# Performance work log

Measured on AMD Instinct MI355X. Metric: run time of the kernel, lower is better.

Reference implementation:

```python
import jax, jax.numpy as jnp
import numpy as np

N_VERTS = 1_000_000
N_EDGES = 3_000_000
H, W = 1024, 1024
MAX_DEPTH = 10.0
DEPTH_SCALE = 1.0
CREGU = 2000.0


def setup_inputs() -> dict:
    key = jax.random.key(0)
    k1, k2, k3, k4, k5, k6 = jax.random.split(key, 6)
    # mesh vertices roughly in a unit-radius blob
    vertices = jax.random.normal(k1, (N_VERTS, 3), dtype=jnp.float32) * 0.5
    vertices_ref = vertices + 0.01 * jax.random.normal(k2, (N_VERTS, 3), dtype=jnp.float32)
    quaternion = jax.random.normal(k3, (4,), dtype=jnp.float32) + jnp.array([0., 0., 0., 1.], jnp.float32)
    translation = jax.random.normal(k4, (3,), dtype=jnp.float32) * 0.05
    hand_image = jax.random.uniform(k5, (H, W), dtype=jnp.float32) * MAX_DEPTH
    # camera per MeshDepthFitterEnergy.setImage: R = diag(1,-1,-1), focal = 2*W
    object_center = np.zeros(3, np.float32)
    object_radius = 0.5
    camera_center = object_center + np.array([-0.5, 0.0, 5.0], np.float32) * object_radius
    R = np.array([[1., 0., 0.], [0., -1., 0.], [0., 0., -1.]], np.float32)
    T = -R.T.dot(camera_center)
    focal = 2.0 * W
    intrinsic = jnp.array([[focal, 0., W / 2.], [0., focal, H / 2.], [0., 0., 1.]], jnp.float32)
    extrinsic = jnp.array(np.column_stack((R, T)), jnp.float32)
    edges = jax.random.randint(k6, (N_EDGES, 2), 0, N_VERTS, dtype=jnp.int64)
    return {"vertices": vertices, "vertices_ref": vertices_ref, "quaternion": quaternion,
            "translation": translation, "hand_image": hand_image,
            "intrinsic": intrinsic, "extrinsic": extrinsic, "edges": edges}


def _qrot(q, v):
    # q: [4] (x,y,z,w) normalized; v: [N,3]
    qvec = q[:3]
    uv = jnp.cross(jnp.broadcast_to(qvec, v.shape), v)
    uuv = jnp.cross(jnp.broadcast_to(qvec, v.shape), uv)
    return v + 2.0 * (q[3] * uv + uuv)


def _forward(vertices, vertices_ref, quaternion, translation, hand_image,
             intrinsic, extrinsic, edges):
    # rigid transform
    q = quaternion / jnp.linalg.norm(quaternion)
    v_centered = vertices - jnp.mean(vertices, axis=0, keepdims=True)
    v_t = _qrot(q, v_centered) + translation  # [N,3]
    # camera projection: P_cam = R x + T ; pix = K P_cam / z
    p_cam = v_t @ extrinsic[:, :3].T + extrinsic[:, 3]  # [N,3]
    proj = p_cam @ intrinsic.T
    z = p_cam[:, 2] * DEPTH_SCALE
    u = proj[:, 0] / proj[:, 2]
    v = proj[:, 1] / proj[:, 2]
    xi = jnp.clip(jnp.round(u), 0, W - 1).astype(jnp.int32)
    yi = jnp.clip(jnp.round(v), 0, H - 1).astype(jnp.int32)
    flat = yi * W + xi  # [N]
    # z-buffer: scatter-min of per-vertex depth (invalid/behind-camera -> MAX_DEPTH)
    zvalid = jnp.where(z > 0, z, MAX_DEPTH)
    depth_flat = jnp.full((H * W,), MAX_DEPTH, dtype=vertices.dtype).at[flat].min(zvalid)
    depth = jnp.clip(depth_flat, 0.0, MAX_DEPTH).reshape(H, W)
    diff_image = (depth - hand_image) ** 2
    e_data = jnp.sum(diff_image)
    # Laplacian rigid energy: cregu * || L (V - Vref) ||^2 over the edge graph
    dv = vertices - vertices_ref
    src, dst = edges[:, 0], edges[:, 1]
    deg = jax.ops.segment_sum(jnp.ones((N_EDGES,), vertices.dtype), src, num_segments=N_VERTS)
    neigh = jax.ops.segment_sum(dv[dst], src, num_segments=N_VERTS)  # [N,3]
    ldv = deg[:, None] * dv - neigh
    e_rigid = CREGU * jnp.sum(ldv ** 2)
    return e_data + e_rigid


def reference(vertices, vertices_ref, quaternion, translation, hand_image,
              intrinsic, extrinsic, edges):
    return _forward(vertices, vertices_ref, quaternion, translation, hand_image,
                    intrinsic, extrinsic, edges)
```

## Files before the change

### kernel.cpp

```cpp
#include <hip/hip_runtime.h>

#define W_IMG 1024
#define H_IMG 1024
#define HW_IMG (W_IMG * H_IMG)
#define NV 1000000
#define NE 3000000
#define NV4 (NE / 2)
#define MAX_DEPTH 10.0f
#define CREGU 2000.0f

#define NBUCKET 245
#define BSHIFT 12
#define BSIZE 4096

#define PREP_BLOCKS 2048
#define HIST_BLOCKS 250
#define HIST_V4 6000
#define SCAT_V4 2048
#define SCAT_EDGES (SCAT_V4 * 2)
#define SCAT_BLOCKS ((NV4 + SCAT_V4 - 1) / SCAT_V4)
#define GEO_BLOCKS 1024
#define TSIZE 2048
#define EDATA_BLOCKS 256

#define QXY 4096.0f
#define IQXY 2.44140625e-4f
#define QZ 2048.0f
#define IQZ 4.8828125e-4f
#define BXY2 1024
#define BZ2 512

typedef int v4i __attribute__((ext_vector_type(4)));

__device__ __forceinline__ unsigned pack_dv32(float x, float y, float z) {
    x = fminf(fmaxf(x, -0.2f), 0.2f);
    y = fminf(fmaxf(y, -0.2f), 0.2f);
    z = fminf(fmaxf(z, -0.2f), 0.2f);
    unsigned px = (unsigned)((int)rintf(x * QXY) + BXY2);
    unsigned py = (unsigned)((int)rintf(y * QXY) + BXY2);
    unsigned pz = (unsigned)((int)rintf(z * QZ) + BZ2);
    return (px << 21) | (py << 10) | pz;
}

__device__ __forceinline__ unsigned long long expand_dv(unsigned p) {
    unsigned long long x = (p >> 21) & 0x7FFu;
    unsigned long long y = (p >> 10) & 0x7FFu;
    unsigned long long z = p & 0x3FFu;
    return (x << 44) | (y << 24) | (z << 6) | 1ull;
}

__device__ __forceinline__ float block_sum_256(float v, float* smem) {
#pragma unroll
    for (int o = 32; o > 0; o >>= 1) v += __shfl_down(v, o, 64);
    int lane = threadIdx.x & 63;
    int wid  = threadIdx.x >> 6;
    if (lane == 0) smem[wid] = v;
    __syncthreads();
    float r = 0.f;
    if (threadIdx.x == 0) r = smem[0] + smem[1] + smem[2] + smem[3];
    __syncthreads();
    return r;
}

__device__ __forceinline__ void prefix245(const unsigned* __restrict__ src,
                                          unsigned* dst) {
    int t = threadIdx.x;
    unsigned h = (t < NBUCKET) ? src[t] : 0u;
    dst[t] = h;
    __syncthreads();
#pragma unroll
    for (int o = 1; o < 256; o <<= 1) {
        unsigned v = (t >= o) ? dst[t - o] : 0u;
        __syncthreads();
        dst[t] += v;
        __syncthreads();
    }
    unsigned excl = dst[t] - h;
    __syncthreads();
    dst[t] = excl;
    __syncthreads();
}

__global__ void k_prep(const float* __restrict__ verts,
                       const float* __restrict__ verts_ref,
                       unsigned* __restrict__ pdv32,
                       unsigned* __restrict__ depth_bits, int ncd,
                       unsigned long long* __restrict__ neigh, int modeA,
                       const v4i* __restrict__ edges2,
                       unsigned* __restrict__ hist,
                       float4* __restrict__ partial) {
    __shared__ float smem[4];
    __shared__ unsigned lh[NBUCKET];
    int i = blockIdx.x * blockDim.x + threadIdx.x;
    int stride = gridDim.x * blockDim.x;

    float sx = 0.f, sy = 0.f, sz = 0.f;
    for (int j = i; j < NV; j += stride) {
        float x = verts[3 * j + 0];
        float y = verts[3 * j + 1];
        float z = verts[3 * j + 2];
        sx += x; sy += y; sz += z;
        pdv32[j] = pack_dv32(x - verts_ref[3 * j + 0],
                             y - verts_ref[3 * j + 1],
                             z - verts_ref[3 * j + 2]);
        if (!modeA) neigh[j] = 0ull;
    }
    size_t totd = (size_t)ncd * HW_IMG;
    for (size_t j = i; j < totd; j += stride) depth_bits[j] = 0x41200000u;

    if (modeA && blockIdx.x < HIST_BLOCKS) {
        for (int t = threadIdx.x; t < NBUCKET; t += blockDim.x) lh[t] = 0u;
        __syncthreads();
        int base = blockIdx.x * HIST_V4;
        for (int k = threadIdx.x; k < HIST_V4; k += blockDim.x) {
            v4i e = __builtin_nontemporal_load(&edges2[base + k]);
            atomicAdd(&lh[(unsigned)e.x >> BSHIFT], 1u);
            atomicAdd(&lh[(unsigned)e.z >> BSHIFT], 1u);
        }
        __syncthreads();
        for (int t = threadIdx.x; t < NBUCKET; t += blockDim.x)
            if (lh[t]) atomicAdd(&hist[t], lh[t]);
    }

    float bx = block_sum_256(sx, smem);
    float by = block_sum_256(sy, smem);
    float bz = block_sum_256(sz, smem);
    if (threadIdx.x == 0) {
        float4 p; p.x = bx; p.y = by; p.z = bz; p.w = 0.f;
        partial[blockIdx.x] = p;
    }
}

union SMem {
    struct {
        unsigned h_key[TSIZE];
        unsigned h_val[TSIZE];
        float rsm[8];
    } geo;
    struct {
        unsigned long long sort[SCAT_EDGES];
        unsigned sLh[NBUCKET];
        unsigned sPfx[256];
        unsigned sDelta[NBUCKET];
        unsigned sOff[256];
    } sc;
};

__global__ void k_main(const v4i* __restrict__ edges2,
                       const unsigned* __restrict__ pdv32,
                       unsigned long long* __restrict__ rec,
                       const unsigned* __restrict__ hist,
                       unsigned* __restrict__ reserve,
                       unsigned long long* __restrict__ neigh, int modeA,
                       const float* __restrict__ verts,
                       const float* __restrict__ quat,
                       const float* __restrict__ trans,
                       const float* __restrict__ intr,
                       const float* __restrict__ extr,
                       const float4* __restrict__ partial,
                       unsigned* __restrict__ depth_bits, int ncd) {
    __shared__ SMem sm;

    if (blockIdx.x >= GEO_BLOCKS) {
        int sb = blockIdx.x - GEO_BLOCKS;
        int base = sb * SCAT_V4;
        if (modeA) {
            for (int t = threadIdx.x; t < NBUCKET; t += blockDim.x) sm.sc.sLh[t] = 0u;
            __syncthreads();

            v4i e[8];
            unsigned r0[8], r1[8];
#pragma unroll
            for (int k = 0; k < 8; ++k) {
                int idx = base + k * 256 + (int)threadIdx.x;
                if (idx < NV4) {
                    e[k] = __builtin_nontemporal_load(&edges2[idx]);
                    r0[k] = atomicAdd(&sm.sc.sLh[(unsigned)e[k].x >> BSHIFT], 1u);
                    r1[k] = atomicAdd(&sm.sc.sLh[(unsigned)e[k].z >> BSHIFT], 1u);
                }
            }
            __syncthreads();
            prefix245(sm.sc.sLh, sm.sc.sPfx);
            prefix245(hist, sm.sc.sOff);
            for (int t = threadIdx.x; t < NBUCKET; t += blockDim.x) {
                unsigned c = sm.sc.sLh[t];
                unsigned res = c ? atomicAdd(&reserve[t], c) : 0u;
                sm.sc.sDelta[t] = sm.sc.sOff[t] + res - sm.sc.sPfx[t];
            }
            __syncthreads();
#pragma unroll
            for (int k = 0; k < 8; ++k) {
                int idx = base + k * 256 + (int)threadIdx.x;
                if (idx < NV4) {
                    unsigned s0 = (unsigned)e[k].x;
                    unsigned b0 = s0 >> BSHIFT;
                    unsigned long long rec0 =
                        ((unsigned long long)b0 << 56) |
                        ((unsigned long long)pdv32[e[k].y] << 12) |
                        (s0 & (BSIZE - 1));
                    sm.sc.sort[sm.sc.sPfx[b0] + r0[k]] = rec0;
                    unsigned s1 = (unsigned)e[k].z;
                    unsigned b1 = s1 >> BSHIFT;
                    unsigned long long rec1 =
                        ((unsigned long long)b1 << 56) |
                        ((unsigned long long)pdv32[e[k].w] << 12) |
                        (s1 & (BSIZE - 1));
                    sm.sc.sort[sm.sc.sPfx[b1] + r1[k]] = rec1;
                }
            }
            __syncthreads();
            int nrec = (base + SCAT_V4 <= NV4) ? SCAT_EDGES
                                               : 2 * (NV4 - base);
#pragma unroll
            for (int k = 0; k < 16; ++k) {
                int t = k * 256 + (int)threadIdx.x;
                if (t < nrec) {
                    unsigned long long r = sm.sc.sort[t];
                    unsigned bin = (unsigned)(r >> 56);
                    rec[(size_t)t + sm.sc.sDelta[bin]] = r;
                }
            }
        } else {
#pragma unroll
            for (int k = 0; k < 8; ++k) {
                int idx = base + k * 256 + (int)threadIdx.x;
                if (idx < NV4) {
                    v4i e = __builtin_nontemporal_load(&edges2[idx]);
                    atomicAdd(&neigh[(size_t)(unsigned)e.x], expand_dv(pdv32[e.y]));
                    atomicAdd(&neigh[(size_t)(unsigned)e.z], expand_dv(pdv32[e.w]));
                }
            }
        }
        return;
    }

    int gb = blockIdx.x;
    for (int s = threadIdx.x; s < TSIZE; s += blockDim.x) {
        sm.geo.h_key[s] = 0xFFFFFFFFu;
        sm.geo.h_val[s] = 0xFFFFFFFFu;
    }
    __syncthreads();

    float sx = 0.f, sy = 0.f, sz = 0.f;
    for (int p = threadIdx.x; p < PREP_BLOCKS; p += blockDim.x) {
        float4 v = partial[p];
        sx += v.x; sy += v.y; sz += v.z;
    }
    float bx = block_sum_256(sx, sm.geo.rsm);
    float by = block_sum_256(sy, sm.geo.rsm);
    float bz = block_sum_256(sz, sm.geo.rsm);
    if (threadIdx.x == 0) {
        const float inv_nv = 1.0f / (float)NV;
        sm.geo.rsm[4] = bx * inv_nv;
        sm.geo.rsm[5] = by * inv_nv;
        sm.geo.rsm[6] = bz * inv_nv;
    }
    __syncthreads();
    float mx = sm.geo.rsm[4], my = sm.geo.rsm[5], mz = sm.geo.rsm[6];

    float qx = quat[0], qy = quat[1], qz = quat[2], qw = quat[3];
    float qn = rsqrtf(qx * qx + qy * qy + qz * qz + qw * qw);
    qx *= qn; qy *= qn; qz *= qn; qw *= qn;
    float t0 = trans[0], t1 = trans[1], t2 = trans[2];
    float e0 = extr[0], e1 = extr[1], e2 = extr[2],  e3 = extr[3];
    float e4 = extr[4], e5 = extr[5], e6 = extr[6],  e7 = extr[7];
    float e8 = extr[8], e9 = extr[9], e10 = extr[10], e11 = extr[11];
    float i0 = intr[0], i1 = intr[1], i2 = intr[2];
    float i3 = intr[3], i4 = intr[4], i5 = intr[5];
    float i6 = intr[6], i7 = intr[7], i8 = intr[8];

    unsigned* __restrict__ db = depth_bits + (size_t)(gb & (ncd - 1)) * HW_IMG;

    int stride = GEO_BLOCKS * blockDim.x;
    for (int j = gb * blockDim.x + threadIdx.x; j < NV; j += stride) {
        float vx = __builtin_nontemporal_load(&verts[3 * j + 0]) - mx;
        float vy = __builtin_nontemporal_load(&verts[3 * j + 1]) - my;
        float vz = __builtin_nontemporal_load(&verts[3 * j + 2]) - mz;

        float uvx = qy * vz - qz * vy;
        float uvy = qz * vx - qx * vz;
        float uvz = qx * vy - qy * vx;
        float uuvx = qy * uvz - qz * uvy;
        float uuvy = qz * uvx - qx * uvz;
        float uuvz = qx * uvy - qy * uvx;
        float tx = vx + 2.f * (qw * uvx + uuvx) + t0;
        float ty = vy + 2.f * (qw * uvy + uuvy) + t1;
        float tz = vz + 2.f * (qw * uvz + uuvz) + t2;

        float px = e0 * tx + e1 * ty + e2  * tz + e3;
        float py = e4 * tx + e5 * ty + e6  * tz + e7;
        float pz = e8 * tx + e9 * ty + e10 * tz + e11;

        float pr0 = i0 * px + i1 * py + i2 * pz;
        float pr1 = i3 * px + i4 * py + i5 * pz;
        float pr2 = i6 * px + i7 * py + i8 * pz;

        float u = pr0 / pr2;
        float v = pr1 / pr2;
        float ru = rintf(u);
        float rv = rintf(v);
        bool border = (ru < 0.f) | (ru > (float)(W_IMG - 1)) |
                      (rv < 0.f) | (rv > (float)(H_IMG - 1));
        float xf = fminf(fmaxf(ru, 0.f), (float)(W_IMG - 1));
        float yf = fminf(fmaxf(rv, 0.f), (float)(H_IMG - 1));
        unsigned flat = (unsigned)((int)yf * W_IMG + (int)xf);

        if (pz > 0.f) {
            unsigned zbits = __float_as_uint(pz);
            bool direct = !border;
            if (border) {
                unsigned slot = (flat * 2654435761u) >> 21;
                bool done = false;
#pragma unroll
                for (int p = 0; p < 4; ++p) {
                    unsigned old = atomicCAS(&sm.geo.h_key[slot], 0xFFFFFFFFu, flat);
                    if (old == 0xFFFFFFFFu || old == flat) {
                        atomicMin(&sm.geo.h_val[slot], zbits);
                        done = true;
                        break;
                    }
                    slot = (slot + 1) & (TSIZE - 1);
                }
                direct = !done;
            }
            if (direct) atomicMin(&db[flat], zbits);
        }
    }
    __syncthreads();
    for (int s = threadIdx.x; s < TSIZE; s += blockDim.x) {
        unsigned k = sm.geo.h_key[s];
        if (k != 0xFFFFFFFFu) atomicMin(&db[k], sm.geo.h_val[s]);
    }
}

__global__ void k_energy(const unsigned* __restrict__ depth_bits, int ncd,
                         const float* __restrict__ hand,
                         const unsigned* __restrict__ pdv32,
                         const unsigned long long* __restrict__ rec,
                         const unsigned* __restrict__ hist,
                         const unsigned long long* __restrict__ neigh, int modeA,
                         float* out) {
    __shared__ unsigned long long acc[BSIZE];
    __shared__ unsigned sOff[256];
    __shared__ float smem[4];

    if (blockIdx.x < NBUCKET) {
        int b = blockIdx.x;
        int vbase = b * BSIZE;
        int nvert = (NV - vbase < BSIZE) ? (NV - vbase) : BSIZE;
        if (modeA) {
            prefix245(hist, sOff);
            unsigned start = sOff[b];
            unsigned count = hist[b];
            for (int v = threadIdx.x; v < BSIZE; v += blockDim.x) acc[v] = 0ull;
            __syncthreads();
            for (unsigned i = threadIdx.x; i < count; i += blockDim.x) {
                unsigned long long r = rec[start + i];
                unsigned p = (unsigned)(r >> 12);
                unsigned s = (unsigned)(r & (BSIZE - 1));
                atomicAdd(&acc[s], expand_dv(p));
            }
            __syncthreads();
        }
        float lacc = 0.f;
        for (int v = threadIdx.x; v < nvert; v += blockDim.x) {
            unsigned long long n = modeA ? acc[v] : neigh[(size_t)vbase + v];
            int cnt = (int)(n & 63ull);
            int rz  = (int)((n >> 6)  & 0x3FFFFull);
            int ry  = (int)((n >> 24) & 0xFFFFFull);
            int rx  = (int)(n >> 44);
            float nx = (float)(rx - cnt * BXY2) * IQXY;
            float ny = (float)(ry - cnt * BXY2) * IQXY;
            float nz = (float)(rz - cnt * BZ2)  * IQZ;
            unsigned p = pdv32[vbase + v];
            float dx = (float)((int)((p >> 21) & 0x7FFu) - BXY2) * IQXY;
            float dy = (float)((int)((p >> 10) & 0x7FFu) - BXY2) * IQXY;
            float dz = (float)((int)(p & 0x3FFu) - BZ2) * IQZ;
            float dg = (float)cnt;
            float lx = dg * dx - nx;
            float ly = dg * dy - ny;
            float lz = dg * dz - nz;
            lacc += lx * lx + ly * ly + lz * lz;
        }
        float bsum = block_sum_256(lacc, smem);
        if (threadIdx.x == 0) atomicAdd(out, CREGU * bsum);
    } else {
        int eb = blockIdx.x - NBUCKET;
        int i = eb * blockDim.x + threadIdx.x;
        int stride = EDATA_BLOCKS * blockDim.x;
        float accd = 0.f;
        for (int j = i; j < HW_IMG; j += stride) {
            float dmin = __uint_as_float(depth_bits[j]);
            for (int c = 1; c < ncd; ++c)
                dmin = fminf(dmin, __uint_as_float(depth_bits[(size_t)c * HW_IMG + j]));
            float depth = fminf(fmaxf(dmin, 0.f), MAX_DEPTH);
            float diff = depth - hand[j];
            accd += diff * diff;
        }
        float bsum = block_sum_256(accd, smem);
        if (threadIdx.x == 0) atomicAdd(out, bsum);
    }
}

extern "C" void kernel_launch(void* const* d_in, const int* in_sizes, int n_in,
                              void* d_out, int out_size, void* d_ws, size_t ws_size,
                              hipStream_t stream) {
    const float* verts     = (const float*)d_in[0];
    const float* verts_ref = (const float*)d_in[1];
    const float* quat      = (const float*)d_in[2];
    const float* trans     = (const float*)d_in[3];
    const float* hand      = (const float*)d_in[4];
    const float* intr      = (const float*)d_in[5];
    const float* extr      = (const float*)d_in[6];
    const int*   edges     = (const int*)d_in[7];
    float* out = (float*)d_out;

    char* ws = (char*)d_ws;
    const size_t OFF_BINS = (size_t)NV * 4;
    const size_t OFF_PART = OFF_BINS + 4096;
    const size_t OFF_REC  = OFF_PART + (size_t)PREP_BLOCKS * 16;

    const size_t A_FIX = OFF_REC + (size_t)NE * 8;
    const size_t B_FIX = OFF_REC + (size_t)NV * 8;

    int modeA, ncd;
    size_t OFF_DEPTH;
    if (ws_size >= A_FIX + 4ull * HW_IMG * 4)      { modeA = 1; ncd = 4; OFF_DEPTH = A_FIX; }
    else if (ws_size >= A_FIX + 2ull * HW_IMG * 4) { modeA = 1; ncd = 2; OFF_DEPTH = A_FIX; }
    else if (ws_size >= A_FIX + 1ull * HW_IMG * 4) { modeA = 1; ncd = 1; OFF_DEPTH = A_FIX; }
    else if (ws_size >= B_FIX + 4ull * HW_IMG * 4) { modeA = 0; ncd = 4; OFF_DEPTH = B_FIX; }
    else if (ws_size >= B_FIX + 2ull * HW_IMG * 4) { modeA = 0; ncd = 2; OFF_DEPTH = B_FIX; }
    else                                           { modeA = 0; ncd = 1; OFF_DEPTH = B_FIX; }

    unsigned*           pdv32      = (unsigned*)ws;
    unsigned*           hist       = (unsigned*)(ws + OFF_BINS);
    unsigned*           reserve    = hist + 256;
    float4*             partial    = (float4*)(ws + OFF_PART);
    unsigned long long* rec        = (unsigned long long*)(ws + OFF_REC);
    unsigned long long* neigh      = (unsigned long long*)(ws + OFF_REC);
    unsigned*           depth_bits = (unsigned*)(ws + OFF_DEPTH);

    const int B = 256;

    hipMemsetAsync(ws + OFF_BINS, 0, 4096, stream);
    hipMemsetAsync(d_out, 0, sizeof(float), stream);

    k_prep<<<PREP_BLOCKS, B, 0, stream>>>(verts, verts_ref, pdv32, depth_bits,
                                          ncd, neigh, modeA, (const v4i*)edges,
                                          hist, partial);
    k_main<<<GEO_BLOCKS + SCAT_BLOCKS, B, 0, stream>>>(
        (const v4i*)edges, pdv32, rec, hist, reserve, neigh, modeA,
        verts, quat, trans, intr, extr, partial, depth_bits, ncd);
    k_energy<<<NBUCKET + EDATA_BLOCKS, B, 0, stream>>>(
        depth_bits, ncd, hand, pdv32, rec, hist, neigh, modeA, out);
}
```

Measured before the change: 234.5 us.

## Vectorize vertex/depth loads, wave-shuffle prefix scan, shrink scatter tiles, add launch bounds

```diff
diff --git a/kernel.cpp b/kernel.cpp
--- a/kernel.cpp
+++ b/kernel.cpp
@@ -14,13 +14,13 @@
 #define BSIZE 4096
 
 #define PREP_BLOCKS 2048
-#define HIST_BLOCKS 250
-#define HIST_V4 6000
-#define SCAT_V4 2048
+#define HIST_BLOCKS 1000
+#define HIST_V4 1500
+#define SCAT_V4 1024
 #define SCAT_EDGES (SCAT_V4 * 2)
 #define SCAT_BLOCKS ((NV4 + SCAT_V4 - 1) / SCAT_V4)
 #define GEO_BLOCKS 1024
-#define TSIZE 2048
+#define TSIZE 1024
 #define EDATA_BLOCKS 256
 
 #define QXY 4096.0f
@@ -31,6 +31,8 @@
 #define BZ2 512
 
 typedef int v4i __attribute__((ext_vector_type(4)));
+typedef float v4f __attribute__((ext_vector_type(4)));
+typedef unsigned v4u __attribute__((ext_vector_type(4)));
 
 __device__ __forceinline__ unsigned pack_dv32(float x, float y, float z) {
     x = fminf(fmaxf(x, -0.2f), 0.2f);
@@ -62,51 +64,65 @@
     return r;
 }
 
-__device__ __forceinline__ void prefix245(const unsigned* __restrict__ src,
-                                          unsigned* dst) {
+__device__ __forceinline__ void prefix245_fast(const unsigned* __restrict__ src,
+                                               unsigned* dst, unsigned* wtmp) {
     int t = threadIdx.x;
+    int lane = t & 63, wid = t >> 6;
     unsigned h = (t < NBUCKET) ? src[t] : 0u;
-    dst[t] = h;
-    __syncthreads();
-#pragma unroll
-    for (int o = 1; o < 256; o <<= 1) {
-        unsigned v = (t >= o) ? dst[t - o] : 0u;
-        __syncthreads();
-        dst[t] += v;
-        __syncthreads();
-    }
-    unsigned excl = dst[t] - h;
-    __syncthreads();
-    dst[t] = excl;
-    __syncthreads();
-}
-
-__global__ void k_prep(const float* __restrict__ verts,
-                       const float* __restrict__ verts_ref,
-                       unsigned* __restrict__ pdv32,
-                       unsigned* __restrict__ depth_bits, int ncd,
-                       unsigned long long* __restrict__ neigh, int modeA,
-                       const v4i* __restrict__ edges2,
-                       unsigned* __restrict__ hist,
-                       float4* __restrict__ partial) {
+    unsigned incl = h;
+#pragma unroll
+    for (int o = 1; o < 64; o <<= 1) {
+        unsigned v = __shfl_up(incl, o, 64);
+        if (lane >= o) incl += v;
+    }
+    if (lane == 63) wtmp[wid] = incl;
+    __syncthreads();
+    unsigned woff = 0u;
+    if (wid > 0) woff += wtmp[0];
+    if (wid > 1) woff += wtmp[1];
+    if (wid > 2) woff += wtmp[2];
+    dst[t] = woff + incl - h;
+    __syncthreads();
+}
+
+__global__ __launch_bounds__(256, 8)
+void k_prep(const float* __restrict__ verts,
+            const float* __restrict__ verts_ref,
+            unsigned* __restrict__ pdv32,
+            unsigned* __restrict__ depth_bits, int ncd,
+            unsigned long long* __restrict__ neigh, int modeA,
+            const v4i* __restrict__ edges2,
+            unsigned* __restrict__ hist,
+            float4* __restrict__ partial) {
     __shared__ float smem[4];
     __shared__ unsigned lh[NBUCKET];
     int i = blockIdx.x * blockDim.x + threadIdx.x;
     int stride = gridDim.x * blockDim.x;
 
     float sx = 0.f, sy = 0.f, sz = 0.f;
-    for (int j = i; j < NV; j += stride) {
-        float x = verts[3 * j + 0];
-        float y = verts[3 * j + 1];
-        float z = verts[3 * j + 2];
-        sx += x; sy += y; sz += z;
-        pdv32[j] = pack_dv32(x - verts_ref[3 * j + 0],
-                             y - verts_ref[3 * j + 1],
-                             z - verts_ref[3 * j + 2]);
-        if (!modeA) neigh[j] = 0ull;
-    }
-    size_t totd = (size_t)ncd * HW_IMG;
-    for (size_t j = i; j < totd; j += stride) depth_bits[j] = 0x41200000u;
+    const int ng = NV / 4;
+    for (int g = i; g < ng; g += stride) {
+        const v4f* vp = (const v4f*)verts + 3 * (size_t)g;
+        const v4f* rp = (const v4f*)verts_ref + 3 * (size_t)g;
+        v4f a = vp[0], b = vp[1], c = vp[2];
+        v4f d = rp[0], e = rp[1], f = rp[2];
+        sx += a.x + a.w + b.z + c.y;
+        sy += a.y + b.x + b.w + c.z;
+        sz += a.z + b.y + c.x + c.w;
+        v4u pk;
+        pk.x = pack_dv32(a.x - d.x, a.y - d.y, a.z - d.z);
+        pk.y = pack_dv32(a.w - d.w, b.x - e.x, b.y - e.y);
+        pk.z = pack_dv32(b.z - e.z, b.w - e.w, c.x - f.x);
+        pk.w = pack_dv32(c.y - f.y, c.z - f.z, c.w - f.w);
+        ((v4u*)pdv32)[g] = pk;
+    }
+    if (!modeA)
+        for (int j = i; j < NV; j += stride) neigh[j] = 0ull;
+
+    size_t totd4 = (size_t)ncd * (HW_IMG / 4);
+    v4u dinit;
+    dinit.x = dinit.y = dinit.z = dinit.w = 0x41200000u;
+    for (size_t j = i; j < totd4; j += stride) ((v4u*)depth_bits)[j] = dinit;
 
     if (modeA && blockIdx.x < HIST_BLOCKS) {
         for (int t = threadIdx.x; t < NBUCKET; t += blockDim.x) lh[t] = 0u;
@@ -141,24 +157,25 @@
         unsigned long long sort[SCAT_EDGES];
         unsigned sLh[NBUCKET];
         unsigned sPfx[256];
-        unsigned sDelta[NBUCKET];
         unsigned sOff[256];
+        unsigned wtmp[4];
     } sc;
 };
 
-__global__ void k_main(const v4i* __restrict__ edges2,
-                       const unsigned* __restrict__ pdv32,
-                       unsigned long long* __restrict__ rec,
-                       const unsigned* __restrict__ hist,
-                       unsigned* __restrict__ reserve,
-                       unsigned long long* __restrict__ neigh, int modeA,
-                       const float* __restrict__ verts,
-                       const float* __restrict__ quat,
-                       const float* __restrict__ trans,
-                       const float* __restrict__ intr,
-                       const float* __restrict__ extr,
-                       const float4* __restrict__ partial,
-                       unsigned* __restrict__ depth_bits, int ncd) {
+__global__ __launch_bounds__(256, 8)
+void k_main(const v4i* __restrict__ edges2,
+            const unsigned* __restrict__ pdv32,
+            unsigned long long* __restrict__ rec,
+            const unsigned* __restrict__ hist,
+            unsigned* __restrict__ reserve,
+            unsigned long long* __restrict__ neigh, int modeA,
+            const float* __restrict__ verts,
+            const float* __restrict__ quat,
+            const float* __restrict__ trans,
+            const float* __restrict__ intr,
+            const float* __restrict__ extr,
+            const float4* __restrict__ partial,
+            unsigned* __restrict__ depth_bits, int ncd) {
     __shared__ SMem sm;
 
     if (blockIdx.x >= GEO_BLOCKS) {
@@ -168,10 +185,10 @@
             for (int t = threadIdx.x; t < NBUCKET; t += blockDim.x) sm.sc.sLh[t] = 0u;
             __syncthreads();
 
-            v4i e[8];
-            unsigned r0[8], r1[8];
-#pragma unroll
-            for (int k = 0; k < 8; ++k) {
+            v4i e[4];
+            unsigned r0[4], r1[4];
+#pragma unroll
+            for (int k = 0; k < 4; ++k) {
                 int idx = base + k * 256 + (int)threadIdx.x;
                 if (idx < NV4) {
                     e[k] = __builtin_nontemporal_load(&edges2[idx]);
@@ -180,16 +197,15 @@
                 }
             }
             __syncthreads();
-            prefix245(sm.sc.sLh, sm.sc.sPfx);
-            prefix245(hist, sm.sc.sOff);
+            prefix245_fast(sm.sc.sLh, sm.sc.sPfx, sm.sc.wtmp);
+            prefix245_fast(hist, sm.sc.sOff, sm.sc.wtmp);
             for (int t = threadIdx.x; t < NBUCKET; t += blockDim.x) {
                 unsigned c = sm.sc.sLh[t];
                 unsigned res = c ? atomicAdd(&reserve[t], c) : 0u;
-                sm.sc.sDelta[t] = sm.sc.sOff[t] + res - sm.sc.sPfx[t];
-            }
-            __syncthreads();
-#pragma unroll
-            for (int k = 0; k < 8; ++k) {
+                sm.sc.sOff[t] += res - sm.sc.sPfx[t];
+            }
+#pragma unroll
+            for (int k = 0; k < 4; ++k) {
                 int idx = base + k * 256 + (int)threadIdx.x;
                 if (idx < NV4) {
                     unsigned s0 = (unsigned)e[k].x;
@@ -212,17 +228,17 @@
             int nrec = (base + SCAT_V4 <= NV4) ? SCAT_EDGES
                                                : 2 * (NV4 - base);
 #pragma unroll
-            for (int k = 0; k < 16; ++k) {
+            for (int k = 0; k < 8; ++k) {
                 int t = k * 256 + (int)threadIdx.x;
                 if (t < nrec) {
                     unsigned long long r = sm.sc.sort[t];
                     unsigned bin = (unsigned)(r >> 56);
-                    rec[(size_t)t + sm.sc.sDelta[bin]] = r;
+                    rec[(size_t)t + sm.sc.sOff[bin]] = r;
                 }
             }
         } else {
 #pragma unroll
-            for (int k = 0; k < 8; ++k) {
+            for (int k = 0; k < 4; ++k) {
                 int idx = base + k * 256 + (int)threadIdx.x;
                 if (idx < NV4) {
                     v4i e = __builtin_nontemporal_load(&edges2[idx]);
@@ -271,59 +287,68 @@
 
     unsigned* __restrict__ db = depth_bits + (size_t)(gb & (ncd - 1)) * HW_IMG;
 
+    const int ng = NV / 4;
     int stride = GEO_BLOCKS * blockDim.x;
-    for (int j = gb * blockDim.x + threadIdx.x; j < NV; j += stride) {
-        float vx = __builtin_nontemporal_load(&verts[3 * j + 0]) - mx;
-        float vy = __builtin_nontemporal_load(&verts[3 * j + 1]) - my;
-        float vz = __builtin_nontemporal_load(&verts[3 * j + 2]) - mz;
-
-        float uvx = qy * vz - qz * vy;
-        float uvy = qz * vx - qx * vz;
-        float uvz = qx * vy - qy * vx;
-        float uuvx = qy * uvz - qz * uvy;
-        float uuvy = qz * uvx - qx * uvz;
-        float uuvz = qx * uvy - qy * uvx;
-        float tx = vx + 2.f * (qw * uvx + uuvx) + t0;
-        float ty = vy + 2.f * (qw * uvy + uuvy) + t1;
-        float tz = vz + 2.f * (qw * uvz + uuvz) + t2;
-
-        float px = e0 * tx + e1 * ty + e2  * tz + e3;
-        float py = e4 * tx + e5 * ty + e6  * tz + e7;
-        float pz = e8 * tx + e9 * ty + e10 * tz + e11;
-
-        float pr0 = i0 * px + i1 * py + i2 * pz;
-        float pr1 = i3 * px + i4 * py + i5 * pz;
-        float pr2 = i6 * px + i7 * py + i8 * pz;
-
-        float u = pr0 / pr2;
-        float v = pr1 / pr2;
-        float ru = rintf(u);
-        float rv = rintf(v);
-        bool border = (ru < 0.f) | (ru > (float)(W_IMG - 1)) |
-                      (rv < 0.f) | (rv > (float)(H_IMG - 1));
-        float xf = fminf(fmaxf(ru, 0.f), (float)(W_IMG - 1));
-        float yf = fminf(fmaxf(rv, 0.f), (float)(H_IMG - 1));
-        unsigned flat = (unsigned)((int)yf * W_IMG + (int)xf);
-
-        if (pz > 0.f) {
-            unsigned zbits = __float_as_uint(pz);
-            bool direct = !border;
-            if (border) {
-                unsigned slot = (flat * 2654435761u) >> 21;
-                bool done = false;
-#pragma unroll
-                for (int p = 0; p < 4; ++p) {
-                    unsigned old = atomicCAS(&sm.geo.h_key[slot], 0xFFFFFFFFu, flat);
-                    if (old == 0xFFFFFFFFu || old == flat) {
-                        atomicMin(&sm.geo.h_val[slot], zbits);
-                        done = true;
-                        break;
+    for (int g = gb * blockDim.x + threadIdx.x; g < ng; g += stride) {
+        const v4f* vp = (const v4f*)verts + 3 * (size_t)g;
+        v4f a = __builtin_nontemporal_load(vp);
+        v4f b = __builtin_nontemporal_load(vp + 1);
+        v4f c = __builtin_nontemporal_load(vp + 2);
+        float gx[4] = {a.x, a.w, b.z, c.y};
+        float gy[4] = {a.y, b.x, b.w, c.z};
+        float gz[4] = {a.z, b.y, c.x, c.w};
+#pragma unroll
+        for (int q = 0; q < 4; ++q) {
+            float vx = gx[q] - mx, vy = gy[q] - my, vz = gz[q] - mz;
+
+            float uvx = qy * vz - qz * vy;
+            float uvy = qz * vx - qx * vz;
+            float uvz = qx * vy - qy * vx;
+            float uuvx = qy * uvz - qz * uvy;
+            float uuvy = qz * uvx - qx * uvz;
+            float uuvz = qx * uvy - qy * uvx;
+            float tx = vx + 2.f * (qw * uvx + uuvx) + t0;
+            float ty = vy + 2.f * (qw * uvy + uuvy) + t1;
+            float tz = vz + 2.f * (qw * uvz + uuvz) + t2;
+
+            float px = e0 * tx + e1 * ty + e2  * tz + e3;
+            float py = e4 * tx + e5 * ty + e6  * tz + e7;
+            float pz = e8 * tx + e9 * ty + e10 * tz + e11;
+
+            float pr0 = i0 * px + i1 * py + i2 * pz;
+            float pr1 = i3 * px + i4 * py + i5 * pz;
+            float pr2 = i6 * px + i7 * py + i8 * pz;
+
+            float u = pr0 / pr2;
+            float v = pr1 / pr2;
+            float ru = rintf(u);
+            float rv = rintf(v);
+            bool border = (ru < 0.f) | (ru > (float)(W_IMG - 1)) |
+                          (rv < 0.f) | (rv > (float)(H_IMG - 1));
+            float xf = fminf(fmaxf(ru, 0.f), (float)(W_IMG - 1));
+            float yf = fminf(fmaxf(rv, 0.f), (float)(H_IMG - 1));
+            unsigned flat = (unsigned)((int)yf * W_IMG + (int)xf);
+
+            if (pz > 0.f) {
+                unsigned zbits = __float_as_uint(pz);
+                bool direct = !border;
+                if (border) {
+                    unsigned slot = (flat * 2654435761u) >> 22;
+                    bool done = false;
+#pragma unroll
+                    for (int p = 0; p < 4; ++p) {
+                        unsigned old = atomicCAS(&sm.geo.h_key[slot], 0xFFFFFFFFu, flat);
+                        if (old == 0xFFFFFFFFu || old == flat) {
+                            atomicMin(&sm.geo.h_val[slot], zbits);
+                            done = true;
+                            break;
+                        }
+                        slot = (slot + 1) & (TSIZE - 1);
                     }
-                    slot = (slot + 1) & (TSIZE - 1);
+                    direct = !done;
                 }
-                direct = !done;
-            }
-            if (direct) atomicMin(&db[flat], zbits);
+                if (direct) atomicMin(&db[flat], zbits);
+            }
         }
     }
     __syncthreads();
@@ -342,6 +367,7 @@
                          float* out) {
     __shared__ unsigned long long acc[BSIZE];
     __shared__ unsigned sOff[256];
+    __shared__ unsigned wtmp[4];
     __shared__ float smem[4];
 
     if (blockIdx.x < NBUCKET) {
@@ -349,7 +375,7 @@
         int vbase = b * BSIZE;
         int nvert = (NV - vbase < BSIZE) ? (NV - vbase) : BSIZE;
         if (modeA) {
-            prefix245(hist, sOff);
+            prefix245_fast(hist, sOff, wtmp);
             unsigned start = sOff[b];
             unsigned count = hist[b];
             for (int v = threadIdx.x; v < BSIZE; v += blockDim.x) acc[v] = 0ull;
@@ -389,13 +415,26 @@
         int i = eb * blockDim.x + threadIdx.x;
         int stride = EDATA_BLOCKS * blockDim.x;
         float accd = 0.f;
-        for (int j = i; j < HW_IMG; j += stride) {
-            float dmin = __uint_as_float(depth_bits[j]);
-            for (int c = 1; c < ncd; ++c)
-                dmin = fminf(dmin, __uint_as_float(depth_bits[(size_t)c * HW_IMG + j]));
-            float depth = fminf(fmaxf(dmin, 0.f), MAX_DEPTH);
-            float diff = depth - hand[j];
-            accd += diff * diff;
+        const int nq = HW_IMG / 4;
+        for (int j = i; j < nq; j += stride) {
+            v4u d0 = ((const v4u*)depth_bits)[j];
+            float m0 = __uint_as_float(d0.x);
+            float m1 = __uint_as_float(d0.y);
+            float m2 = __uint_as_float(d0.z);
+            float m3 = __uint_as_float(d0.w);
+            for (int c = 1; c < ncd; ++c) {
+                v4u dc = ((const v4u*)(depth_bits + (size_t)c * HW_IMG))[j];
+                m0 = fminf(m0, __uint_as_float(dc.x));
+                m1 = fminf(m1, __uint_as_float(dc.y));
+                m2 = fminf(m2, __uint_as_float(dc.z));
+                m3 = fminf(m3, __uint_as_float(dc.w));
+            }
+            v4f h = ((const v4f*)hand)[j];
+            float f0 = fminf(fmaxf(m0, 0.f), MAX_DEPTH) - h.x;
+            float f1 = fminf(fmaxf(m1, 0.f), MAX_DEPTH) - h.y;
+            float f2 = fminf(fmaxf(m2, 0.f), MAX_DEPTH) - h.z;
+            float f3 = fminf(fmaxf(m3, 0.f), MAX_DEPTH) - h.w;
+            accd += f0 * f0 + f1 * f1 + f2 * f2 + f3 * f3;
         }
         float bsum = block_sum_256(accd, smem);
         if (threadIdx.x == 0) atomicAdd(out, bsum);
```

After: 253.3 us. 1.08x slower.
